# Kernel optimization log

Measured on AMD Instinct MI355X. Metric: run time of the kernel, lower is better.

The kernel has to match this reference:

```python
import jax, jax.numpy as jnp
import numpy as np

B, N, C = 16, 1024, 256
NH, DH = 8, 32          # dense attention heads
NHD, P = 8, 4           # deformable heads / sampling points
Hs = Ws = 32            # value spatial grid (N == Hs*Ws)
HID = 1024              # mlp hidden = 4*C


def setup_inputs() -> dict:
    key = jax.random.key(0)
    ks = jax.random.split(key, 16)
    rn = lambda i, shape, s=1.0: jax.random.normal(ks[i], shape, jnp.float32) * s
    return {
        "x": rn(0, (B, N, C)),
        "ref": jax.random.uniform(ks[1], (B, N, 2), jnp.float32),
        "value": rn(2, (B, N, C)),
        "ln1_w": jnp.ones((C,), jnp.float32), "ln1_b": jnp.zeros((C,), jnp.float32),
        "ln2_w": jnp.ones((C,), jnp.float32), "ln2_b": jnp.zeros((C,), jnp.float32),
        "ln3_w": jnp.ones((C,), jnp.float32), "ln3_b": jnp.zeros((C,), jnp.float32),
        "qkv_w": rn(3, (3 * C, C), 0.05),
        "proj_w": rn(4, (C, C), 0.05), "proj_b": jnp.zeros((C,), jnp.float32),
        "off_w": rn(5, (NHD * P * 2, C), 0.01), "off_b": rn(6, (NHD * P * 2,), 0.5),
        "aw_w": rn(7, (NHD * P, C), 0.01), "aw_b": jnp.zeros((NHD * P,), jnp.float32),
        "vproj_w": rn(8, (C, C), 0.05), "vproj_b": jnp.zeros((C,), jnp.float32),
        "oproj_w": rn(9, (C, C), 0.05), "oproj_b": jnp.zeros((C,), jnp.float32),
        "fc1_w": rn(10, (HID, C), 0.05), "fc1_b": jnp.zeros((HID,), jnp.float32),
        "fc2_w": rn(11, (C, HID), 0.05), "fc2_b": jnp.zeros((C,), jnp.float32),
    }


def _ln(x, w, b):
    m = x.mean(-1, keepdims=True)
    v = ((x - m) ** 2).mean(-1, keepdims=True)
    return (x - m) * jax.lax.rsqrt(v + 1e-5) * w + b


def _attn(x, qkv_w, proj_w, proj_b):
    qkv = (x @ qkv_w.T).reshape(B, N, 3, NH, DH)
    q, k, v = qkv[:, :, 0], qkv[:, :, 1], qkv[:, :, 2]
    a = jnp.einsum('bqhd,bkhd->bhqk', q, k) * (DH ** -0.5)
    a = jax.nn.softmax(a, axis=-1)
    o = jnp.einsum('bhqk,bkhd->bqhd', a, v).reshape(B, N, C)
    return o @ proj_w.T + proj_b


def _deform(q, ref, value, off_w, off_b, aw_w, aw_b, vproj_w, vproj_b, oproj_w, oproj_b):
    # single-level MS deformable attention (Deformable-DETR style)
    v = (value @ vproj_w.T + vproj_b).reshape(B, Hs * Ws, NHD, DH)
    off = (q @ off_w.T + off_b).reshape(B, N, NHD, P, 2)
    aw = jax.nn.softmax((q @ aw_w.T + aw_b).reshape(B, N, NHD, P), axis=-1)
    norm = jnp.array([Ws, Hs], jnp.float32)
    loc = ref[:, :, None, None, :] + off / norm  # [B,N,NHD,P,2] normalized coords
    gx = loc[..., 0] * Ws - 0.5
    gy = loc[..., 1] * Hs - 0.5
    x0 = jnp.floor(gx); y0 = jnp.floor(gy)
    lx = gx - x0; ly = gy - y0
    x0i = x0.astype(jnp.int32); y0i = y0.astype(jnp.int32)
    b_idx = jnp.arange(B)[:, None, None, None]
    h_idx = jnp.arange(NHD)[None, None, :, None]

    def gather(xi, yi):
        valid = ((xi >= 0) & (xi < Ws) & (yi >= 0) & (yi < Hs)).astype(jnp.float32)
        idx = jnp.clip(yi, 0, Hs - 1) * Ws + jnp.clip(xi, 0, Ws - 1)
        return v[b_idx, idx, h_idx] * valid[..., None]  # [B,N,NHD,P,DH]

    s = (gather(x0i, y0i) * ((1 - lx) * (1 - ly))[..., None]
         + gather(x0i + 1, y0i) * (lx * (1 - ly))[..., None]
         + gather(x0i, y0i + 1) * ((1 - lx) * ly)[..., None]
         + gather(x0i + 1, y0i + 1) * (lx * ly)[..., None])
    out = (s * aw[..., None]).sum(axis=3).reshape(B, N, C)
    return out @ oproj_w.T + oproj_b


def reference(x, ref, value, ln1_w, ln1_b, ln2_w, ln2_b, ln3_w, ln3_b,
              qkv_w, proj_w, proj_b, off_w, off_b, aw_w, aw_b,
              vproj_w, vproj_b, oproj_w, oproj_b, fc1_w, fc1_b, fc2_w, fc2_b):
    x = x + _attn(_ln(x, ln1_w, ln1_b), qkv_w, proj_w, proj_b)
    x = x + _deform(_ln(x, ln2_w, ln2_b), ref, value,
                    off_w, off_b, aw_w, aw_b, vproj_w, vproj_b, oproj_w, oproj_b)
    h = jax.nn.gelu(_ln(x, ln3_w, ln3_b) @ fc1_w.T + fc1_b, approximate=False) @ fc2_w.T + fc2_b
    return x + h
```

## Files before the change

kernel.cpp:

```cpp
#include <hip/hip_runtime.h>
#include <hip/hip_bf16.h>

#define Bq   16
#define Nq   1024
#define Cq   256
#define NHq  8
#define DHq  32
#define HIDq 1024
#define BNq  (Bq * Nq)

typedef float f32x4 __attribute__((ext_vector_type(4)));
typedef short bf16x8 __attribute__((ext_vector_type(8)));
typedef unsigned short ushort_t;

__device__ __forceinline__ unsigned int f2bf(float f) {
    unsigned int u = __builtin_bit_cast(unsigned int, f);
    u = (u + 0x7fffu + ((u >> 16) & 1u)) >> 16;
    return u & 0xffffu;
}
__device__ __forceinline__ unsigned int packbf2(float a, float b) {
    unsigned int ua = __builtin_bit_cast(unsigned int, a) + 0x8000u;
    unsigned int ub = __builtin_bit_cast(unsigned int, b) + 0x8000u;
    return __builtin_amdgcn_perm(ub, ua, 0x07060302);
}
__device__ __forceinline__ float gelu_t(float x) {
    float y = x * (0.7978845608028654f + 0.035677408136300125f * x * x);
    float e = __builtin_amdgcn_exp2f(y * 2.8853900817779268f);
    return x - x / (1.f + e);
}

typedef __attribute__((address_space(1))) const unsigned int* gas_u32;
typedef __attribute__((address_space(3))) unsigned int* las_u32;
__device__ __forceinline__ void gload16(const void* g, void* l) {
    __builtin_amdgcn_global_load_lds((gas_u32)g, (las_u32)l, 16, 0, 0);
}

struct CastSeg { const float* src; ushort_t* dst; int nblk; int n; };
struct CastArgs { CastSeg s[9]; };

__global__ __launch_bounds__(256) void castm(CastArgs a) {
    int bid = blockIdx.x;
    int seg = 0, acc = 0;
    for (seg = 0; seg < 9; seg++) {
        if (bid < acc + a.s[seg].nblk) break;
        acc += a.s[seg].nblk;
    }
    const CastSeg sg = a.s[seg];
    int i = (bid - acc) * 1024 + threadIdx.x * 4;
    if (i < sg.n) {
        float4 v = *(const float4*)(sg.src + i);
        uint2 u;
        u.x = packbf2(v.x, v.y);
        u.y = packbf2(v.z, v.w);
        *(uint2*)(sg.dst + i) = u;
    }
}

__global__ __launch_bounds__(256) void ln_kernel(const float* __restrict__ X,
                                                 const float* __restrict__ w,
                                                 const float* __restrict__ b,
                                                 ushort_t* __restrict__ Y) {
    int wave = threadIdx.x >> 6, lane = threadIdx.x & 63;
    int t = blockIdx.x * 4 + wave;
    float4 v = *(const float4*)(X + (size_t)t * Cq + lane * 4);
    float s = v.x + v.y + v.z + v.w;
#pragma unroll
    for (int d = 1; d < 64; d <<= 1) s += __shfl_xor(s, d);
    float mean = s * (1.f / 256.f);
    float4 dv = {v.x - mean, v.y - mean, v.z - mean, v.w - mean};
    float q = dv.x * dv.x + dv.y * dv.y + dv.z * dv.z + dv.w * dv.w;
#pragma unroll
    for (int d = 1; d < 64; d <<= 1) q += __shfl_xor(q, d);
    float rs = rsqrtf(q * (1.f / 256.f) + 1e-5f);
    float4 wv = *(const float4*)(w + lane * 4);
    float4 bv = *(const float4*)(b + lane * 4);
    uint2 u;
    u.x = packbf2(dv.x * rs * wv.x + bv.x, dv.y * rs * wv.y + bv.y);
    u.y = packbf2(dv.z * rs * wv.z + bv.z, dv.w * rs * wv.w + bv.w);
    *(uint2*)(Y + (size_t)t * Cq + lane * 4) = u;
}

template <int OMODE, bool GELU_, bool RESID, int KT>
__global__ __launch_bounds__(256) void mgemm(const ushort_t* __restrict__ A,
                                             const ushort_t* __restrict__ W,
                                             const float* __restrict__ bias,
                                             const float* __restrict__ R,
                                             void* __restrict__ OutP,
                                             int M, int Nn) {
    __shared__ __align__(16) ushort_t Al[8192];
    __shared__ __align__(16) ushort_t Bl[8192];
    int m0 = blockIdx.x * 128, n0 = blockIdx.y * 128;
    int tid = threadIdx.x;
    int w = tid >> 6, lane = tid & 63;
    int l15 = lane & 15, quad = lane >> 4;
    int wrow = w >> 1, wcol = w & 1;

    f32x4 acc[4][4];
#pragma unroll
    for (int i = 0; i < 4; i++)
#pragma unroll
        for (int j = 0; j < 4; j++) acc[i][j] = (f32x4){0.f, 0.f, 0.f, 0.f};

    const ushort_t* gA0 = A + (size_t)(m0 + lane) * KT + w * 8;
    const ushort_t* gA1 = A + (size_t)(m0 + 64 + lane) * KT + w * 8;
    const ushort_t* gB0 = W + (size_t)(n0 + lane) * KT + w * 8;
    const ushort_t* gB1 = W + (size_t)(n0 + 64 + lane) * KT + w * 8;
    ushort_t* lA0  = &Al[(w * 128) * 8];
    ushort_t* lA1  = &Al[(w * 128 + 64) * 8];
    ushort_t* lA0h = &Al[((w + 4) * 128) * 8];
    ushort_t* lA1h = &Al[((w + 4) * 128 + 64) * 8];
    ushort_t* lB0  = &Bl[(w * 128) * 8];
    ushort_t* lB1  = &Bl[(w * 128 + 64) * 8];
    ushort_t* lB0h = &Bl[((w + 4) * 128) * 8];
    ushort_t* lB1h = &Bl[((w + 4) * 128 + 64) * 8];

#pragma unroll
    for (int k0 = 0; k0 < KT; k0 += 64) {
        gload16(gA0 + k0, lA0);
        gload16(gA1 + k0, lA1);
        gload16(gA0 + k0 + 32, lA0h);
        gload16(gA1 + k0 + 32, lA1h);
        gload16(gB0 + k0, lB0);
        gload16(gB1 + k0, lB1);
        gload16(gB0 + k0 + 32, lB0h);
        gload16(gB1 + k0 + 32, lB1h);
        __syncthreads();

#pragma unroll
        for (int ks = 0; ks < 2; ks++) {
            bf16x8 aF[4], bF[4];
#pragma unroll
            for (int i = 0; i < 4; i++)
                aF[i] = *(const bf16x8*)&Al[((ks * 4 + quad) * 128 + wrow * 64 + i * 16 + l15) * 8];
#pragma unroll
            for (int j = 0; j < 4; j++)
                bF[j] = *(const bf16x8*)&Bl[((ks * 4 + quad) * 128 + wcol * 64 + j * 16 + l15) * 8];
#pragma unroll
            for (int i = 0; i < 4; i++)
#pragma unroll
                for (int j = 0; j < 4; j++)
                    acc[i][j] = __builtin_amdgcn_mfma_f32_16x16x32_bf16(bF[j], aF[i], acc[i][j], 0, 0, 0);
        }
        __syncthreads();
    }

#pragma unroll
    for (int i = 0; i < 4; i++) {
        int mg = m0 + wrow * 64 + i * 16 + l15;
#pragma unroll
        for (int j = 0; j < 4; j++) {
            int ng = n0 + wcol * 64 + j * 16 + quad * 4;
            f32x4 rv = acc[i][j];
            if constexpr (OMODE == 1) {
                int which = ng >> 8;
                int h = (ng >> 5) & 7;
                int d = ng & 31;
                int bb = mg >> 10, nn = mg & 1023;
                ushort_t* qb = (ushort_t*)OutP;
                if (which == 2) {
                    size_t dst = 2 * (size_t)BNq * Cq +
                                 ((size_t)(bb * 8 + h) * 32 + d) * 1024 + nn;
#pragma unroll
                    for (int r = 0; r < 4; r++)
                        qb[dst + (size_t)r * 1024] = (ushort_t)f2bf(rv[r]);
                } else {
                    if (which == 0) {
                        const float sc = 0.17677669529663687f * 1.4426950408889634f;
                        rv[0] *= sc; rv[1] *= sc; rv[2] *= sc; rv[3] *= sc;
                    }
                    size_t dst = (size_t)which * ((size_t)BNq * Cq) +
                                 ((size_t)(bb * 8 + h) * 1024 + nn) * 32 + d;
                    uint2 pk;
                    pk.x = packbf2(rv[0], rv[1]);
                    pk.y = packbf2(rv[2], rv[3]);
                    *(uint2*)(qb + dst) = pk;
                }
            } else if constexpr (OMODE == 3) {
                if (ng >= 96) continue;
                if (ng < 64) {
                    float4 bv = *(const float4*)(bias + ng);
                    rv[0] += bv.x; rv[1] += bv.y; rv[2] += bv.z; rv[3] += bv.w;
                    *(float4*)((float*)OutP + (size_t)mg * 64 + ng) =
                        make_float4(rv[0], rv[1], rv[2], rv[3]);
                } else {
                    float4 bv = *(const float4*)(R + (ng - 64));
                    rv[0] += bv.x; rv[1] += bv.y; rv[2] += bv.z; rv[3] += bv.w;
                    *(float4*)((float*)OutP + (size_t)BNq * 64 + (size_t)mg * 32 + (ng - 64)) =
                        make_float4(rv[0], rv[1], rv[2], rv[3]);
                }
            } else {
                if (bias) {
                    float4 bv = *(const float4*)(bias + ng);
                    rv[0] += bv.x; rv[1] += bv.y; rv[2] += bv.z; rv[3] += bv.w;
                }
                if (GELU_) {
#pragma unroll
                    for (int r = 0; r < 4; r++) rv[r] = gelu_t(rv[r]);
                }
                if constexpr (OMODE == 2) {
                    uint2 pk;
                    pk.x = packbf2(rv[0], rv[1]);
                    pk.y = packbf2(rv[2], rv[3]);
                    *(uint2*)((ushort_t*)OutP + (size_t)mg * Nn + ng) = pk;
                } else {
                    if (RESID) {
                        float4 rr = *(const float4*)(R + (size_t)mg * Nn + ng);
                        rv[0] += rr.x; rv[1] += rr.y; rv[2] += rr.z; rv[3] += rr.w;
                    }
                    *(float4*)((float*)OutP + (size_t)mg * Nn + ng) =
                        make_float4(rv[0], rv[1], rv[2], rv[3]);
                }
            }
        }
    }
}

__global__ __launch_bounds__(256) void attn_mfma(const ushort_t* __restrict__ Qb,
                                                 const ushort_t* __restrict__ Kb,
                                                 const ushort_t* __restrict__ Vtg,
                                                 ushort_t* __restrict__ o) {
    int bh = blockIdx.x;
    int b = bh >> 3, h = bh & 7;
    int q0 = blockIdx.y * 128;
    int tid = threadIdx.x;
    int wave = tid >> 6, lane = tid & 63;
    int l15 = lane & 15, quad = lane >> 4;

    __shared__ __align__(16) ushort_t Ks[64][40];
    __shared__ __align__(16) ushort_t Vs[32][88];
    __shared__ __align__(16) ushort_t Ps[4][32][72];

    const size_t hb = (size_t)bh * 32768;

    bf16x8 qfrag[2];
#pragma unroll
    for (int g = 0; g < 2; g++)
        qfrag[g] = *(const bf16x8*)(Qb + hb + (size_t)(q0 + wave * 32 + g * 16 + l15) * 32 + quad * 8);

    f32x4 oa[2][2];
#pragma unroll
    for (int g = 0; g < 2; g++)
#pragma unroll
        for (int t = 0; t < 2; t++) oa[g][t] = (f32x4){0.f, 0.f, 0.f, 0.f};
    float lsum[2] = {0.f, 0.f};

    int krow = tid >> 2, kch = tid & 3;
    int vrow = tid >> 3, vch = tid & 7;
    const ushort_t* kgp = Kb + hb + (size_t)krow * 32 + kch * 8;
    const ushort_t* vgp = Vtg + hb + (size_t)vrow * 1024 + vch * 8;

    for (int kt = 0; kt < 16; kt++) {
        __syncthreads();
        *(bf16x8*)&Ks[krow][kch * 8] = *(const bf16x8*)(kgp + kt * 64 * 32);
        *(bf16x8*)&Vs[vrow][vch * 8] = *(const bf16x8*)(vgp + kt * 64);
        __syncthreads();

        bf16x8 kf[4];
#pragma unroll
        for (int kg = 0; kg < 4; kg++)
            kf[kg] = *(const bf16x8*)&Ks[kg * 16 + l15][quad * 8];

        const f32x4 z = {0.f, 0.f, 0.f, 0.f};
#pragma unroll
        for (int g = 0; g < 2; g++) {
#pragma unroll
            for (int kg = 0; kg < 4; kg++) {
                f32x4 st = __builtin_amdgcn_mfma_f32_16x16x32_bf16(kf[kg], qfrag[g], z, 0, 0, 0);
                float e0 = __builtin_amdgcn_exp2f(st[0]);
                float e1 = __builtin_amdgcn_exp2f(st[1]);
                float e2 = __builtin_amdgcn_exp2f(st[2]);
                float e3 = __builtin_amdgcn_exp2f(st[3]);
                lsum[g] += (e0 + e1) + (e2 + e3);
                uint2 pk;
                pk.x = packbf2(e0, e1);
                pk.y = packbf2(e2, e3);
                *(uint2*)&Ps[wave][g * 16 + l15][kg * 16 + quad * 4] = pk;
            }
        }
#pragma unroll
        for (int c = 0; c < 2; c++) {
            bf16x8 vb0 = *(const bf16x8*)&Vs[l15][c * 32 + quad * 8];
            bf16x8 vb1 = *(const bf16x8*)&Vs[16 + l15][c * 32 + quad * 8];
#pragma unroll
            for (int g = 0; g < 2; g++) {
                bf16x8 pa = *(const bf16x8*)&Ps[wave][g * 16 + l15][c * 32 + quad * 8];
                oa[g][0] = __builtin_amdgcn_mfma_f32_16x16x32_bf16(pa, vb0, oa[g][0], 0, 0, 0);
                oa[g][1] = __builtin_amdgcn_mfma_f32_16x16x32_bf16(pa, vb1, oa[g][1], 0, 0, 0);
            }
        }
    }

#pragma unroll
    for (int g = 0; g < 2; g++) {
        float rs = lsum[g];
        rs += __shfl_xor(rs, 16);
        rs += __shfl_xor(rs, 32);
        lsum[g] = rs;
    }
#pragma unroll
    for (int g = 0; g < 2; g++) {
#pragma unroll
        for (int r = 0; r < 4; r++) {
            float inv = 1.f / __shfl(lsum[g], quad * 4 + r);
            int q = q0 + wave * 32 + g * 16 + quad * 4 + r;
            ushort_t* orow = o + ((size_t)(b * 1024 + q)) * 256 + h * 32;
            orow[l15] = (ushort_t)f2bf(oa[g][0][r] * inv);
            orow[l15 + 16] = (ushort_t)f2bf(oa[g][1][r] * inv);
        }
    }
}

__global__ __launch_bounds__(256) void deform_kernel(const float* __restrict__ ref,
                                                     const float* __restrict__ off,
                                                     const float* __restrict__ awl,
                                                     const float* __restrict__ v,
                                                     ushort_t* __restrict__ out) {
    int t = blockIdx.x;
    int b = t >> 10;
    int tid = threadIdx.x;
    int h = tid >> 5, d = tid & 31;

    float rx = ref[(size_t)t * 2 + 0];
    float ry = ref[(size_t)t * 2 + 1];
    const float* offr = off + (size_t)t * 64 + h * 8;
    const float* awr = awl + (size_t)t * 32 + h * 4;

    float L0 = awr[0], L1 = awr[1], L2 = awr[2], L3 = awr[3];
    float mm = fmaxf(fmaxf(L0, L1), fmaxf(L2, L3));
    float e0 = __expf(L0 - mm), e1 = __expf(L1 - mm), e2 = __expf(L2 - mm), e3 = __expf(L3 - mm);
    float inv = 1.f / (e0 + e1 + e2 + e3);
    float aw[4] = {e0 * inv, e1 * inv, e2 * inv, e3 * inv};

    const float* vb = v + (size_t)b * Nq * Cq + h * 32 + d;

    float s = 0.f;
#pragma unroll
    for (int p = 0; p < 4; p++) {
        float gx = rx * 32.f + offr[p * 2 + 0] - 0.5f;
        float gy = ry * 32.f + offr[p * 2 + 1] - 0.5f;
        float x0f = floorf(gx), y0f = floorf(gy);
        float lx = gx - x0f, ly = gy - y0f;
        int x0 = (int)x0f, y0 = (int)y0f;
        auto g = [&](int xi, int yi) -> float {
            if (xi < 0 || xi > 31 || yi < 0 || yi > 31) return 0.f;
            return vb[(size_t)(yi * 32 + xi) * Cq];
        };
        float sp = g(x0, y0) * (1.f - lx) * (1.f - ly)
                 + g(x0 + 1, y0) * lx * (1.f - ly)
                 + g(x0, y0 + 1) * (1.f - lx) * ly
                 + g(x0 + 1, y0 + 1) * lx * ly;
        s += aw[p] * sp;
    }
    out[(size_t)t * Cq + h * 32 + d] = (ushort_t)f2bf(s);
}

extern "C" void kernel_launch(void* const* d_in, const int* in_sizes, int n_in,
                              void* d_out, int out_size, void* d_ws, size_t ws_size,
                              hipStream_t stream) {
    const size_t S = (size_t)BNq * Cq;
    float* ws = (float*)d_ws;
    float* X = ws;
    ushort_t* Ybf = (ushort_t*)(ws + S);
    ushort_t* Wbf = (ushort_t*)(ws + S + S / 2);

    ushort_t* Wqkv   = Wbf;
    ushort_t* Wproj  = Wbf + 196608;
    ushort_t* Woff   = Wbf + 262144;
    ushort_t* Waw    = Wbf + 278528;
    ushort_t* Wvproj = Wbf + 286720;
    ushort_t* Woproj = Wbf + 352256;
    ushort_t* Wfc1   = Wbf + 417792;
    ushort_t* Wfc2   = Wbf + 679936;

    ushort_t* QKVbf = (ushort_t*)(ws + 2 * S);
    ushort_t* O1bf  = (ushort_t*)(ws + 2 * S + 3 * S / 2);
    float* Vb   = ws + 2 * S + S / 2;
    float* OffB = ws + 2 * S + 3 * S / 2;
    float* AwB  = OffB + (size_t)BNq * 64;
    ushort_t* Sbbf = (ushort_t*)(AwB + (size_t)BNq * 32);
    ushort_t* Hbbf = (ushort_t*)(ws + 2 * S);
    ushort_t* Valbf = (ushort_t*)(ws + 9 * S / 2);

    auto fp = [&](int i) { return (const float*)d_in[i]; };
    const float* x_in = fp(0);

    CastArgs ca;
    ca.s[0] = {fp(9),  Wqkv,   192, 196608};
    ca.s[1] = {fp(10), Wproj,  64,  65536};
    ca.s[2] = {fp(12), Woff,   16,  16384};
    ca.s[3] = {fp(14), Waw,    8,   8192};
    ca.s[4] = {fp(16), Wvproj, 64,  65536};
    ca.s[5] = {fp(18), Woproj, 64,  65536};
    ca.s[6] = {fp(20), Wfc1,   256, 262144};
    ca.s[7] = {fp(22), Wfc2,   256, 262144};
    ca.s[8] = {fp(2),  Valbf,  4096, (int)S};
    castm<<<5016, 256, 0, stream>>>(ca);

    ln_kernel<<<BNq / 4, 256, 0, stream>>>(x_in, fp(3), fp(4), Ybf);
    mgemm<1, false, false, 256><<<dim3(128, 6), 256, 0, stream>>>(
        Ybf, Wqkv, nullptr, nullptr, QKVbf, BNq, 768);
    attn_mfma<<<dim3(128, 8), 256, 0, stream>>>(
        QKVbf, QKVbf + S, QKVbf + 2 * S, O1bf);
    mgemm<0, false, true, 256><<<dim3(128, 2), 256, 0, stream>>>(
        O1bf, Wproj, fp(11), x_in, X, BNq, 256);

    ln_kernel<<<BNq / 4, 256, 0, stream>>>(X, fp(5), fp(6), Ybf);
    mgemm<0, false, false, 256><<<dim3(128, 2), 256, 0, stream>>>(
        Valbf, Wvproj, fp(17), nullptr, Vb, BNq, 256);
    mgemm<3, false, false, 256><<<dim3(128, 1), 256, 0, stream>>>(
        Ybf, Woff, fp(13), fp(15), OffB, BNq, 96);
    deform_kernel<<<BNq, 256, 0, stream>>>(fp(1), OffB, AwB, Vb, Sbbf);
    mgemm<0, false, true, 256><<<dim3(128, 2), 256, 0, stream>>>(
        Sbbf, Woproj, fp(19), X, X, BNq, 256);

    ln_kernel<<<BNq / 4, 256, 0, stream>>>(X, fp(7), fp(8), Ybf);
    mgemm<2, true, false, 256><<<dim3(128, 8), 256, 0, stream>>>(
        Ybf, Wfc1, fp(21), nullptr, Hbbf, BNq, 1024);
    mgemm<0, false, true, 1024><<<dim3(128, 2), 256, 0, stream>>>(
        Hbbf, Wfc2, fp(23), X, d_out, BNq, 256);
}
```

Baseline: 342.6 us.

## Store residual stream and deform values in bf16, use 64-wide N tiles for narrow GEMMs

The residual stream X and the projected deformable values are now stored as bf16 instead of fp32. The LayerNorm, deform gather and residual epilogues read bf16 and widen it in registers, which halves the memory traffic of these intermediates. The GEMM kernel takes the N tile width as a template parameter, and the 256- and 96-wide output GEMMs use 64-wide tiles to launch twice as many blocks. Keeping the residual in bf16 adds rounding error that builds up across the three residual additions.

```diff
diff --git a/kernel.cpp b/kernel.cpp
--- a/kernel.cpp
+++ b/kernel.cpp
@@ -23,6 +23,8 @@
     unsigned int ub = __builtin_bit_cast(unsigned int, b) + 0x8000u;
     return __builtin_amdgcn_perm(ub, ua, 0x07060302);
 }
+__device__ __forceinline__ float bflo(unsigned int u) { return __builtin_bit_cast(float, u << 16); }
+__device__ __forceinline__ float bfhi(unsigned int u) { return __builtin_bit_cast(float, u & 0xffff0000u); }
 __device__ __forceinline__ float gelu_t(float x) {
     float y = x * (0.7978845608028654f + 0.035677408136300125f * x * x);
     float e = __builtin_amdgcn_exp2f(y * 2.8853900817779268f);
@@ -56,13 +58,20 @@
     }
 }
 
-__global__ __launch_bounds__(256) void ln_kernel(const float* __restrict__ X,
+template <typename TI>
+__global__ __launch_bounds__(256) void ln_kernel(const TI* __restrict__ X,
                                                  const float* __restrict__ w,
                                                  const float* __restrict__ b,
                                                  ushort_t* __restrict__ Y) {
     int wave = threadIdx.x >> 6, lane = threadIdx.x & 63;
     int t = blockIdx.x * 4 + wave;
-    float4 v = *(const float4*)(X + (size_t)t * Cq + lane * 4);
+    float4 v;
+    if constexpr (sizeof(TI) == 4) {
+        v = *(const float4*)((const float*)X + (size_t)t * Cq + lane * 4);
+    } else {
+        uint2 u = *(const uint2*)((const ushort_t*)X + (size_t)t * Cq + lane * 4);
+        v = make_float4(bflo(u.x), bfhi(u.x), bflo(u.y), bfhi(u.y));
+    }
     float s = v.x + v.y + v.z + v.w;
 #pragma unroll
     for (int d = 1; d < 64; d <<= 1) s += __shfl_xor(s, d);
@@ -80,39 +89,40 @@
     *(uint2*)(Y + (size_t)t * Cq + lane * 4) = u;
 }
 
-template <int OMODE, bool GELU_, bool RESID, int KT>
+template <int OMODE, bool GELU_, bool RESID, int KT, int NT, typename RT>
 __global__ __launch_bounds__(256) void mgemm(const ushort_t* __restrict__ A,
                                              const ushort_t* __restrict__ W,
                                              const float* __restrict__ bias,
-                                             const float* __restrict__ R,
+                                             const void* __restrict__ R,
                                              void* __restrict__ OutP,
                                              int M, int Nn) {
+    constexpr int NJ = NT / 32;
     __shared__ __align__(16) ushort_t Al[8192];
-    __shared__ __align__(16) ushort_t Bl[8192];
-    int m0 = blockIdx.x * 128, n0 = blockIdx.y * 128;
+    __shared__ __align__(16) ushort_t Bl[NT * 64];
+    int m0 = blockIdx.x * 128, n0 = blockIdx.y * NT;
     int tid = threadIdx.x;
     int w = tid >> 6, lane = tid & 63;
     int l15 = lane & 15, quad = lane >> 4;
     int wrow = w >> 1, wcol = w & 1;
 
-    f32x4 acc[4][4];
+    f32x4 acc[4][NJ];
 #pragma unroll
     for (int i = 0; i < 4; i++)
 #pragma unroll
-        for (int j = 0; j < 4; j++) acc[i][j] = (f32x4){0.f, 0.f, 0.f, 0.f};
+        for (int j = 0; j < NJ; j++) acc[i][j] = (f32x4){0.f, 0.f, 0.f, 0.f};
 
     const ushort_t* gA0 = A + (size_t)(m0 + lane) * KT + w * 8;
     const ushort_t* gA1 = A + (size_t)(m0 + 64 + lane) * KT + w * 8;
     const ushort_t* gB0 = W + (size_t)(n0 + lane) * KT + w * 8;
-    const ushort_t* gB1 = W + (size_t)(n0 + 64 + lane) * KT + w * 8;
+    const ushort_t* gB1 = (NT == 128) ? W + (size_t)(n0 + 64 + lane) * KT + w * 8 : nullptr;
     ushort_t* lA0  = &Al[(w * 128) * 8];
     ushort_t* lA1  = &Al[(w * 128 + 64) * 8];
     ushort_t* lA0h = &Al[((w + 4) * 128) * 8];
     ushort_t* lA1h = &Al[((w + 4) * 128 + 64) * 8];
-    ushort_t* lB0  = &Bl[(w * 128) * 8];
-    ushort_t* lB1  = &Bl[(w * 128 + 64) * 8];
-    ushort_t* lB0h = &Bl[((w + 4) * 128) * 8];
-    ushort_t* lB1h = &Bl[((w + 4) * 128 + 64) * 8];
+    ushort_t* lB0  = &Bl[(w * NT) * 8];
+    ushort_t* lB0h = &Bl[((w + 4) * NT) * 8];
+    ushort_t* lB1  = (NT == 128) ? &Bl[(w * NT + 64) * 8] : nullptr;
+    ushort_t* lB1h = (NT == 128) ? &Bl[((w + 4) * NT + 64) * 8] : nullptr;
 
 #pragma unroll
     for (int k0 = 0; k0 < KT; k0 += 64) {
@@ -121,24 +131,26 @@
         gload16(gA0 + k0 + 32, lA0h);
         gload16(gA1 + k0 + 32, lA1h);
         gload16(gB0 + k0, lB0);
-        gload16(gB1 + k0, lB1);
         gload16(gB0 + k0 + 32, lB0h);
-        gload16(gB1 + k0 + 32, lB1h);
+        if constexpr (NT == 128) {
+            gload16(gB1 + k0, lB1);
+            gload16(gB1 + k0 + 32, lB1h);
+        }
         __syncthreads();
 
 #pragma unroll
         for (int ks = 0; ks < 2; ks++) {
-            bf16x8 aF[4], bF[4];
+            bf16x8 aF[4], bF[NJ];
 #pragma unroll
             for (int i = 0; i < 4; i++)
                 aF[i] = *(const bf16x8*)&Al[((ks * 4 + quad) * 128 + wrow * 64 + i * 16 + l15) * 8];
 #pragma unroll
-            for (int j = 0; j < 4; j++)
-                bF[j] = *(const bf16x8*)&Bl[((ks * 4 + quad) * 128 + wcol * 64 + j * 16 + l15) * 8];
+            for (int j = 0; j < NJ; j++)
+                bF[j] = *(const bf16x8*)&Bl[((ks * 4 + quad) * NT + wcol * (NT / 2) + j * 16 + l15) * 8];
 #pragma unroll
             for (int i = 0; i < 4; i++)
 #pragma unroll
-                for (int j = 0; j < 4; j++)
+                for (int j = 0; j < NJ; j++)
                     acc[i][j] = __builtin_amdgcn_mfma_f32_16x16x32_bf16(bF[j], aF[i], acc[i][j], 0, 0, 0);
         }
         __syncthreads();
@@ -148,8 +160,8 @@
     for (int i = 0; i < 4; i++) {
         int mg = m0 + wrow * 64 + i * 16 + l15;
 #pragma unroll
-        for (int j = 0; j < 4; j++) {
-            int ng = n0 + wcol * 64 + j * 16 + quad * 4;
+        for (int j = 0; j < NJ; j++) {
+            int ng = n0 + wcol * (NT / 2) + j * 16 + quad * 4;
             f32x4 rv = acc[i][j];
             if constexpr (OMODE == 1) {
                 int which = ng >> 8;
@@ -183,7 +195,7 @@
                     *(float4*)((float*)OutP + (size_t)mg * 64 + ng) =
                         make_float4(rv[0], rv[1], rv[2], rv[3]);
                 } else {
-                    float4 bv = *(const float4*)(R + (ng - 64));
+                    float4 bv = *(const float4*)((const float*)R + (ng - 64));
                     rv[0] += bv.x; rv[1] += bv.y; rv[2] += bv.z; rv[3] += bv.w;
                     *(float4*)((float*)OutP + (size_t)BNq * 64 + (size_t)mg * 32 + (ng - 64)) =
                         make_float4(rv[0], rv[1], rv[2], rv[3]);
@@ -196,6 +208,16 @@
                 if (GELU_) {
 #pragma unroll
                     for (int r = 0; r < 4; r++) rv[r] = gelu_t(rv[r]);
+                }
+                if (RESID) {
+                    if constexpr (sizeof(RT) == 4) {
+                        float4 rr = *(const float4*)((const float*)R + (size_t)mg * Nn + ng);
+                        rv[0] += rr.x; rv[1] += rr.y; rv[2] += rr.z; rv[3] += rr.w;
+                    } else {
+                        uint2 ru = *(const uint2*)((const ushort_t*)R + (size_t)mg * Nn + ng);
+                        rv[0] += bflo(ru.x); rv[1] += bfhi(ru.x);
+                        rv[2] += bflo(ru.y); rv[3] += bfhi(ru.y);
+                    }
                 }
                 if constexpr (OMODE == 2) {
                     uint2 pk;
@@ -203,10 +225,6 @@
                     pk.y = packbf2(rv[2], rv[3]);
                     *(uint2*)((ushort_t*)OutP + (size_t)mg * Nn + ng) = pk;
                 } else {
-                    if (RESID) {
-                        float4 rr = *(const float4*)(R + (size_t)mg * Nn + ng);
-                        rv[0] += rr.x; rv[1] += rr.y; rv[2] += rr.z; rv[3] += rr.w;
-                    }
                     *(float4*)((float*)OutP + (size_t)mg * Nn + ng) =
                         make_float4(rv[0], rv[1], rv[2], rv[3]);
                 }
@@ -313,7 +331,7 @@
 __global__ __launch_bounds__(256) void deform_kernel(const float* __restrict__ ref,
                                                      const float* __restrict__ off,
                                                      const float* __restrict__ awl,
-                                                     const float* __restrict__ v,
+                                                     const ushort_t* __restrict__ v,
                                                      ushort_t* __restrict__ out) {
     int t = blockIdx.x;
     int b = t >> 10;
@@ -331,7 +349,7 @@
     float inv = 1.f / (e0 + e1 + e2 + e3);
     float aw[4] = {e0 * inv, e1 * inv, e2 * inv, e3 * inv};
 
-    const float* vb = v + (size_t)b * Nq * Cq + h * 32 + d;
+    const ushort_t* vb = v + (size_t)b * Nq * Cq + h * 32 + d;
 
     float s = 0.f;
 #pragma unroll
@@ -343,7 +361,7 @@
         int x0 = (int)x0f, y0 = (int)y0f;
         auto g = [&](int xi, int yi) -> float {
             if (xi < 0 || xi > 31 || yi < 0 || yi > 31) return 0.f;
-            return vb[(size_t)(yi * 32 + xi) * Cq];
+            return bflo((unsigned int)vb[(size_t)(yi * 32 + xi) * Cq]);
         };
         float sp = g(x0, y0) * (1.f - lx) * (1.f - ly)
                  + g(x0 + 1, y0) * lx * (1.f - ly)
@@ -359,14 +377,13 @@
                               hipStream_t stream) {
     const size_t S = (size_t)BNq * Cq;
     float* ws = (float*)d_ws;
-    float* X = ws;
-    ushort_t* Ybf = (ushort_t*)(ws + S);
-    ushort_t* Wbf = (ushort_t*)(ws + S + S / 2);
+    ushort_t* Xbf = (ushort_t*)ws;
+    ushort_t* Ybf = (ushort_t*)(ws + S / 2);
+    ushort_t* Wbf = (ushort_t*)(ws + S);
 
     ushort_t* Wqkv   = Wbf;
     ushort_t* Wproj  = Wbf + 196608;
     ushort_t* Woff   = Wbf + 262144;
-    ushort_t* Waw    = Wbf + 278528;
     ushort_t* Wvproj = Wbf + 286720;
     ushort_t* Woproj = Wbf + 352256;
     ushort_t* Wfc1   = Wbf + 417792;
@@ -374,10 +391,10 @@
 
     ushort_t* QKVbf = (ushort_t*)(ws + 2 * S);
     ushort_t* O1bf  = (ushort_t*)(ws + 2 * S + 3 * S / 2);
-    float* Vb   = ws + 2 * S + S / 2;
-    float* OffB = ws + 2 * S + 3 * S / 2;
+    ushort_t* Vbbf  = (ushort_t*)(ws + 2 * S);
+    float* OffB = ws + 2 * S + S / 2;
     float* AwB  = OffB + (size_t)BNq * 64;
-    ushort_t* Sbbf = (ushort_t*)(AwB + (size_t)BNq * 32);
+    ushort_t* Sbbf = (ushort_t*)(ws + 3 * S);
     ushort_t* Hbbf = (ushort_t*)(ws + 2 * S);
     ushort_t* Valbf = (ushort_t*)(ws + 9 * S / 2);
 
@@ -388,7 +405,7 @@
     ca.s[0] = {fp(9),  Wqkv,   192, 196608};
     ca.s[1] = {fp(10), Wproj,  64,  65536};
     ca.s[2] = {fp(12), Woff,   16,  16384};
-    ca.s[3] = {fp(14), Waw,    8,   8192};
+    ca.s[3] = {fp(14), Wbf + 278528, 8, 8192};
     ca.s[4] = {fp(16), Wvproj, 64,  65536};
     ca.s[5] = {fp(18), Woproj, 64,  65536};
     ca.s[6] = {fp(20), Wfc1,   256, 262144};
@@ -396,26 +413,26 @@
     ca.s[8] = {fp(2),  Valbf,  4096, (int)S};
     castm<<<5016, 256, 0, stream>>>(ca);
 
-    ln_kernel<<<BNq / 4, 256, 0, stream>>>(x_in, fp(3), fp(4), Ybf);
-    mgemm<1, false, false, 256><<<dim3(128, 6), 256, 0, stream>>>(
+    ln_kernel<float><<<BNq / 4, 256, 0, stream>>>(x_in, fp(3), fp(4), Ybf);
+    mgemm<1, false, false, 256, 128, float><<<dim3(128, 6), 256, 0, stream>>>(
         Ybf, Wqkv, nullptr, nullptr, QKVbf, BNq, 768);
     attn_mfma<<<dim3(128, 8), 256, 0, stream>>>(
         QKVbf, QKVbf + S, QKVbf + 2 * S, O1bf);
-    mgemm<0, false, true, 256><<<dim3(128, 2), 256, 0, stream>>>(
-        O1bf, Wproj, fp(11), x_in, X, BNq, 256);
-
-    ln_kernel<<<BNq / 4, 256, 0, stream>>>(X, fp(5), fp(6), Ybf);
-    mgemm<0, false, false, 256><<<dim3(128, 2), 256, 0, stream>>>(
-        Valbf, Wvproj, fp(17), nullptr, Vb, BNq, 256);
-    mgemm<3, false, false, 256><<<dim3(128, 1), 256, 0, stream>>>(
+    mgemm<2, false, true, 256, 64, float><<<dim3(128, 4), 256, 0, stream>>>(
+        O1bf, Wproj, fp(11), x_in, Xbf, BNq, 256);
+
+    ln_kernel<ushort_t><<<BNq / 4, 256, 0, stream>>>(Xbf, fp(5), fp(6), Ybf);
+    mgemm<2, false, false, 256, 64, float><<<dim3(128, 4), 256, 0, stream>>>(
+        Valbf, Wvproj, fp(17), nullptr, Vbbf, BNq, 256);
+    mgemm<3, false, false, 256, 64, float><<<dim3(128, 2), 256, 0, stream>>>(
         Ybf, Woff, fp(13), fp(15), OffB, BNq, 96);
-    deform_kernel<<<BNq, 256, 0, stream>>>(fp(1), OffB, AwB, Vb, Sbbf);
-    mgemm<0, false, true, 256><<<dim3(128, 2), 256, 0, stream>>>(
-        Sbbf, Woproj, fp(19), X, X, BNq, 256);
-
-    ln_kernel<<<BNq / 4, 256, 0, stream>>>(X, fp(7), fp(8), Ybf);
-    mgemm<2, true, false, 256><<<dim3(128, 8), 256, 0, stream>>>(
+    deform_kernel<<<BNq, 256, 0, stream>>>(fp(1), OffB, AwB, Vbbf, Sbbf);
+    mgemm<2, false, true, 256, 64, ushort_t><<<dim3(128, 4), 256, 0, stream>>>(
+        Sbbf, Woproj, fp(19), Xbf, Xbf, BNq, 256);
+
+    ln_kernel<ushort_t><<<BNq / 4, 256, 0, stream>>>(Xbf, fp(7), fp(8), Ybf);
+    mgemm<2, true, false, 256, 128, float><<<dim3(128, 8), 256, 0, stream>>>(
         Ybf, Wfc1, fp(21), nullptr, Hbbf, BNq, 1024);
-    mgemm<0, false, true, 1024><<<dim3(128, 2), 256, 0, stream>>>(
-        Hbbf, Wfc2, fp(23), X, d_out, BNq, 256);
-}
+    mgemm<0, false, true, 1024, 64, ushort_t><<<dim3(128, 4), 256, 0, stream>>>(
+        Hbbf, Wfc2, fp(23), Xbf, d_out, BNq, 256);
+}
```

New measurement: 357.6 us. +4.4%, slower.
